# Performance work log

Measured on AMD Instinct MI355X. Metric: run time of the kernel, lower is better.

The kernel has to match this reference:

```python
import jax, jax.numpy as jnp
import numpy as np

BSZ, D = 64, 65536
N_NODES, N_FEATS, EMBED_DIM = 1024, 256, 256


def setup_inputs() -> dict:
    key = jax.random.key(0)
    k1, k2, k3, k4, k5, k6 = jax.random.split(key, 6)
    flat_inputs = jax.random.normal(k1, (BSZ, D), dtype=jnp.float32)
    node_ids = jax.random.randint(k2, (BSZ, D), 0, N_NODES, dtype=jnp.int64 if jax.config.jax_enable_x64 else jnp.int32)
    feat_ids = jax.random.randint(k3, (BSZ, D), 0, N_FEATS, dtype=jnp.int64 if jax.config.jax_enable_x64 else jnp.int32)
    # Linear(n_feats -> embed_dim): W is (embed_dim, n_feats) like torch, plus bias.
    lim = 1.0 / np.sqrt(N_FEATS)
    W = jax.random.uniform(k4, (EMBED_DIM, N_FEATS), minval=-lim, maxval=lim, dtype=jnp.float32)
    b = jax.random.uniform(k5, (EMBED_DIM,), minval=-lim, maxval=lim, dtype=jnp.float32)
    global_emb = jax.random.normal(k6, (N_NODES, EMBED_DIM), dtype=jnp.float32)
    return {"flat_inputs": flat_inputs, "node_ids": node_ids, "feat_ids": feat_ids,
            "W": W, "b": b, "global_emb": global_emb}


def _expand(vals, node_ids, feat_ids, n_nodes, n_feats):
    # scatter-fill a dense (bsz, n_nodes, n_feats) tensor (zeros elsewhere)
    bsz, d = vals.shape
    batch_ids = jnp.broadcast_to(jnp.arange(bsz)[:, None], (bsz, d))
    out = jnp.zeros((bsz, n_nodes, n_feats), dtype=vals.dtype)
    return out.at[batch_ids.ravel(), node_ids.ravel(), feat_ids.ravel()].set(vals.ravel())


def reference(flat_inputs, node_ids, feat_ids, W, b, global_emb):
    obs_mat = _expand(flat_inputs, node_ids, feat_ids, N_NODES, N_FEATS)
    mask_mat = _expand(jnp.ones_like(flat_inputs), node_ids, feat_ids, N_NODES, N_FEATS)
    obs_counts = mask_mat.sum(-1, keepdims=True)            # (bsz, n_nodes, 1)
    obs_masked = jnp.nan_to_num((obs_mat * mask_mat) / obs_counts)
    missing_node_mask = obs_counts == 0
    # nodewise Linear + global embedding broadcast over batch
    embedded = jnp.einsum('bnf,ef->bne', obs_masked, W) + b + global_emb[None, :, :]
    return embedded, missing_node_mask
```

## Files before the change

kernel.cpp:

```cpp
#include <hip/hip_runtime.h>
#include <hip/hip_bf16.h>

#define BSZ    64
#define DLEN   65536
#define NNODES 1024
#define NFEATS 256
#define EDIM   256
#define NROWS  (BSZ * NNODES)

#define NRANGE  32
#define NBUCKET (BSZ * NRANGE)
#define CHUNK   2048
#define LCAP    112
#define GCAP    2304
#define WPAD    268
#define HROWS   32

typedef __bf16 bf16x8 __attribute__((ext_vector_type(8)));
typedef float  f32x4  __attribute__((ext_vector_type(4)));

__device__ __forceinline__ unsigned short f2bf(float x) {
  union { float f; unsigned u; } c; c.f = x;
  unsigned r = c.u + 0x7FFFu + ((c.u >> 16) & 1u);
  return (unsigned short)(r >> 16);
}

__global__ __launch_bounds__(256) void wconv_kernel(
    const float* __restrict__ W, unsigned short* __restrict__ Wb,
    unsigned* __restrict__ gcnt) {
  int i = (blockIdx.x * 256 + threadIdx.x) * 4;
  float4 w = *(const float4*)(W + i);
  ushort4 o;
  o.x = f2bf(w.x); o.y = f2bf(w.y); o.z = f2bf(w.z); o.w = f2bf(w.w);
  *(ushort4*)(Wb + i) = o;
  if (blockIdx.x < 2)
    ((uint4*)gcnt)[blockIdx.x * 256 + threadIdx.x] = make_uint4(0u, 0u, 0u, 0u);
}

__global__ __launch_bounds__(512, 8) void bucket_kernel(
    const float* __restrict__ x, const int* __restrict__ nid,
    const int* __restrict__ fid, unsigned* __restrict__ gcnt,
    uint2* __restrict__ gbuf) {
  __shared__ uint2 lbuf[NRANGE][LCAP];
  __shared__ unsigned lcnt[NRANGE];
  __shared__ unsigned lbase[NRANGE];

  const int t = threadIdx.x;
  if (t < NRANGE) lcnt[t] = 0;
  __syncthreads();

  const int b = blockIdx.x >> 5;
  const int i = blockIdx.x * CHUNK + t * 4;

  float4 xv = *(const float4*)(x + i);
  int4   nv = *(const int4*)(nid + i);
  int4   fv = *(const int4*)(fid + i);
  int   nd[4] = {nv.x, nv.y, nv.z, nv.w};
  int   ft[4] = {fv.x, fv.y, fv.z, fv.w};
  float vl[4] = {xv.x, xv.y, xv.z, xv.w};
#pragma unroll
  for (int j = 0; j < 4; ++j) {
    int d = (i + j) & 0xFFFF;
    unsigned pack = (((unsigned)(d + 1)) << 15) | ((unsigned)f2bf(vl[j]) >> 1);
    int r = nd[j] >> 5;
    uint2 rec;
    rec.x = pack;
    rec.y = (unsigned)((nd[j] & 31) * WPAD + ft[j]);
    unsigned li = atomicAdd(&lcnt[r], 1u);
    if (li < LCAP) {
      lbuf[r][li] = rec;
    } else {
      unsigned gi = atomicAdd(&gcnt[b * NRANGE + r], 1u);
      if (gi < GCAP) gbuf[(size_t)(b * NRANGE + r) * GCAP + gi] = rec;
    }
  }
  __syncthreads();

  if (t < NRANGE) {
    unsigned n = lcnt[t]; if (n > LCAP) n = LCAP;
    lcnt[t] = n;
    lbase[t] = atomicAdd(&gcnt[b * NRANGE + t], n);
  }
  __syncthreads();

  const int wv = t >> 6, lane = t & 63;
#pragma unroll
  for (int rr = 0; rr < 4; ++rr) {
    int r = wv * 4 + rr;
    unsigned n  = lcnt[r];
    unsigned bs = lbase[r];
    uint2* dst = gbuf + (size_t)(b * NRANGE + r) * GCAP;
    for (unsigned j = lane; j < n; j += 64) {
      unsigned gi = bs + j;
      if (gi < GCAP) dst[gi] = lbuf[r][j];
    }
  }
}

__global__ __launch_bounds__(512, 8) void fused_kernel(
    const unsigned* __restrict__ gcnt, const uint2* __restrict__ gbuf,
    const unsigned short* __restrict__ Wb, const float* __restrict__ bias,
    const float* __restrict__ gemb,
    float* __restrict__ out_emb, float* __restrict__ out_mask) {
  __shared__ __align__(16) unsigned win[HROWS * WPAD];
  __shared__ float scl[HROWS];

  const int t = threadIdx.x;
  const int g = blockIdx.x;
  const int row0 = g * HROWS;
  const int nb = (g & 31) * HROWS;

  uint4* wz = (uint4*)win;
  for (int j = t; j < (HROWS * WPAD) / 4; j += 512) wz[j] = make_uint4(0u, 0u, 0u, 0u);
  __syncthreads();

  int cn = (int)gcnt[g]; if (cn > GCAP) cn = GCAP;
  const uint2* bk = gbuf + (size_t)g * GCAP;
  const uint4* bk4 = (const uint4*)bk;
  int np = cn >> 1;
  {
    uint4 r0, r1, r2;
    bool v0 = t < np, v1 = t + 512 < np, v2 = t + 1024 < np;
    if (v0) r0 = bk4[t];
    if (v1) r1 = bk4[t + 512];
    if (v2) r2 = bk4[t + 1024];
    if (v0) { atomicMax(&win[r0.y], r0.x); atomicMax(&win[r0.w], r0.z); }
    if (v1) { atomicMax(&win[r1.y], r1.x); atomicMax(&win[r1.w], r1.z); }
    if (v2) { atomicMax(&win[r2.y], r2.x); atomicMax(&win[r2.w], r2.z); }
    if ((cn & 1) && t == 0) {
      uint2 rec = bk[cn - 1];
      atomicMax(&win[rec.y], rec.x);
    }
  }
  __syncthreads();

  {
    const int lr  = t >> 4;
    const int seg = t & 15;
    const uint4* rowp = (const uint4*)&win[lr * WPAD];
    int c = 0;
#pragma unroll
    for (int j = 0; j < 4; ++j) {
      uint4 w = rowp[seg + 16 * j];
      c += (w.x != 0u) + (w.y != 0u) + (w.z != 0u) + (w.w != 0u);
    }
    c += __shfl_down(c, 8, 16);
    c += __shfl_down(c, 4, 16);
    c += __shfl_down(c, 2, 16);
    c += __shfl_down(c, 1, 16);
    if (seg == 0) {
      scl[lr] = c ? 1.0f / (float)c : 0.0f;
      out_mask[row0 + lr] = c ? 0.0f : 1.0f;
    }
  }

  const int wv   = t >> 6;
  const int lane = t & 63;
  const int cl   = lane & 15;
  const int q    = lane >> 4;
  const int col0 = wv * 32;

  f32x4 acc[2][2];
#pragma unroll
  for (int mt = 0; mt < 2; ++mt)
#pragma unroll
    for (int nt = 0; nt < 2; ++nt) acc[mt][nt] = (f32x4)(0.0f);

#pragma unroll
  for (int ks = 0; ks < 8; ++ks) {
    bf16x8 bfr[2];
#pragma unroll
    for (int nt = 0; nt < 2; ++nt) {
      const uint4* wp = (const uint4*)(Wb + (size_t)(col0 + nt * 16 + cl) * NFEATS + ks * 32 + q * 8);
      bfr[nt] = __builtin_bit_cast(bf16x8, *wp);
    }
#pragma unroll
    for (int mt = 0; mt < 2; ++mt) {
      const uint4* ap = (const uint4*)&win[(mt * 16 + cl) * WPAD + ks * 32 + q * 8];
      uint4 lo = ap[0], hi = ap[1];
      uint4 pk;
      pk.x = ((lo.x & 0x7FFFu) << 1) | ((lo.y & 0x7FFFu) << 17);
      pk.y = ((lo.z & 0x7FFFu) << 1) | ((lo.w & 0x7FFFu) << 17);
      pk.z = ((hi.x & 0x7FFFu) << 1) | ((hi.y & 0x7FFFu) << 17);
      pk.w = ((hi.z & 0x7FFFu) << 1) | ((hi.w & 0x7FFFu) << 17);
      bf16x8 afr = __builtin_bit_cast(bf16x8, pk);
#pragma unroll
      for (int nt = 0; nt < 2; ++nt)
        acc[mt][nt] = __builtin_amdgcn_mfma_f32_16x16x32_bf16(afr, bfr[nt], acc[mt][nt], 0, 0, 0);
    }
  }
  __syncthreads();

#pragma unroll
  for (int nt = 0; nt < 2; ++nt) {
    int col = col0 + nt * 16 + cl;
    float bv = bias[col];
#pragma unroll
    for (int mt = 0; mt < 2; ++mt) {
#pragma unroll
      for (int r2 = 0; r2 < 4; ++r2) {
        int row = mt * 16 + q * 4 + r2;
        float o = acc[mt][nt][r2] * scl[row] + bv + gemb[(size_t)(nb + row) * EDIM + col];
        out_emb[(size_t)(row0 + row) * EDIM + col] = o;
      }
    }
  }
}

extern "C" void kernel_launch(void* const* d_in, const int* in_sizes, int n_in,
                              void* d_out, int out_size, void* d_ws, size_t ws_size,
                              hipStream_t stream) {
  const float* x    = (const float*)d_in[0];
  const int*   nid  = (const int*)d_in[1];
  const int*   fid  = (const int*)d_in[2];
  const float* W    = (const float*)d_in[3];
  const float* bias = (const float*)d_in[4];
  const float* gemb = (const float*)d_in[5];

  float* out_emb  = (float*)d_out;
  float* out_mask = out_emb + (size_t)NROWS * EDIM;

  unsigned* gcnt = (unsigned*)d_ws;
  uint2* gbuf = (uint2*)((char*)d_ws + 8192);
  unsigned short* Wb = (unsigned short*)((char*)d_ws + 8192 + (size_t)NBUCKET * GCAP * sizeof(uint2));

  wconv_kernel<<<64, 256, 0, stream>>>(W, Wb, gcnt);
  bucket_kernel<<<(BSZ * DLEN) / CHUNK, 512, 0, stream>>>(x, nid, fid, gcnt, gbuf);
  fused_kernel<<<NBUCKET, 512, 0, stream>>>(gcnt, gbuf, Wb, bias, gemb, out_emb, out_mask);
}
```

Baseline: 159.9 us.

## Replace bucketing with direct global atomicMax into output buffer as scratch

The two-level bucket pipeline (shared-memory staging, then per-bucket global buffers, then shared-memory atomics) is replaced. The output embedding buffer is first zeroed and used as a dense (batch, node, feat) scratch grid. A scatter kernel then does one global atomicMax per input element into that grid, and the GEMM kernel loads its 32-row tile back into shared memory before overwriting the same rows with results. This removes the bucket counters, overflow handling and the intermediate record buffer. In exchange it adds a full-size zero pass and a full-size read-back of the output tensor, and it spreads 4M atomics across a grid far larger than L2.

```diff
diff --git a/kernel.cpp b/kernel.cpp
--- a/kernel.cpp
+++ b/kernel.cpp
@@ -8,13 +8,10 @@
 #define EDIM   256
 #define NROWS  (BSZ * NNODES)
 
-#define NRANGE  32
-#define NBUCKET (BSZ * NRANGE)
-#define CHUNK   2048
-#define LCAP    112
-#define GCAP    2304
-#define WPAD    268
-#define HROWS   32
+#define WPAD   268
+#define HROWS  32
+#define NBLK   (NROWS / HROWS)
+
 
 typedef __bf16 bf16x8 __attribute__((ext_vector_type(8)));
 typedef float  f32x4  __attribute__((ext_vector_type(4)));
@@ -25,80 +22,46 @@
   return (unsigned short)(r >> 16);
 }
 
-__global__ __launch_bounds__(256) void wconv_kernel(
+__global__ __launch_bounds__(256) void zero_wconv_kernel(
     const float* __restrict__ W, unsigned short* __restrict__ Wb,
-    unsigned* __restrict__ gcnt) {
-  int i = (blockIdx.x * 256 + threadIdx.x) * 4;
-  float4 w = *(const float4*)(W + i);
-  ushort4 o;
-  o.x = f2bf(w.x); o.y = f2bf(w.y); o.z = f2bf(w.z); o.w = f2bf(w.w);
-  *(ushort4*)(Wb + i) = o;
-  if (blockIdx.x < 2)
-    ((uint4*)gcnt)[blockIdx.x * 256 + threadIdx.x] = make_uint4(0u, 0u, 0u, 0u);
+    uint4* __restrict__ owin) {
+  const int t = threadIdx.x;
+  const int base = blockIdx.x * 1024 + t;
+#pragma unroll
+  for (int k = 0; k < 4; ++k)
+    owin[base + k * 256] = make_uint4(0u, 0u, 0u, 0u);
+  if (blockIdx.x < 64) {
+    int i = (blockIdx.x * 256 + t) * 4;
+    float4 w = *(const float4*)(W + i);
+    ushort4 o;
+    o.x = f2bf(w.x); o.y = f2bf(w.y); o.z = f2bf(w.z); o.w = f2bf(w.w);
+    *(ushort4*)(Wb + i) = o;
+  }
 }
 
-__global__ __launch_bounds__(512, 8) void bucket_kernel(
+__global__ __launch_bounds__(512, 8) void scatter_kernel(
     const float* __restrict__ x, const int* __restrict__ nid,
-    const int* __restrict__ fid, unsigned* __restrict__ gcnt,
-    uint2* __restrict__ gbuf) {
-  __shared__ uint2 lbuf[NRANGE][LCAP];
-  __shared__ unsigned lcnt[NRANGE];
-  __shared__ unsigned lbase[NRANGE];
-
+    const int* __restrict__ fid, unsigned* __restrict__ win) {
   const int t = threadIdx.x;
-  if (t < NRANGE) lcnt[t] = 0;
-  __syncthreads();
-
-  const int b = blockIdx.x >> 5;
-  const int i = blockIdx.x * CHUNK + t * 4;
+  const int i = (blockIdx.x * 512 + t) * 4;
 
   float4 xv = *(const float4*)(x + i);
   int4   nv = *(const int4*)(nid + i);
   int4   fv = *(const int4*)(fid + i);
+  const unsigned bb = (((unsigned)i >> 16) << 18);
   int   nd[4] = {nv.x, nv.y, nv.z, nv.w};
   int   ft[4] = {fv.x, fv.y, fv.z, fv.w};
   float vl[4] = {xv.x, xv.y, xv.z, xv.w};
 #pragma unroll
   for (int j = 0; j < 4; ++j) {
-    int d = (i + j) & 0xFFFF;
-    unsigned pack = (((unsigned)(d + 1)) << 15) | ((unsigned)f2bf(vl[j]) >> 1);
-    int r = nd[j] >> 5;
-    uint2 rec;
-    rec.x = pack;
-    rec.y = (unsigned)((nd[j] & 31) * WPAD + ft[j]);
-    unsigned li = atomicAdd(&lcnt[r], 1u);
-    if (li < LCAP) {
-      lbuf[r][li] = rec;
-    } else {
-      unsigned gi = atomicAdd(&gcnt[b * NRANGE + r], 1u);
-      if (gi < GCAP) gbuf[(size_t)(b * NRANGE + r) * GCAP + gi] = rec;
-    }
-  }
-  __syncthreads();
-
-  if (t < NRANGE) {
-    unsigned n = lcnt[t]; if (n > LCAP) n = LCAP;
-    lcnt[t] = n;
-    lbase[t] = atomicAdd(&gcnt[b * NRANGE + t], n);
-  }
-  __syncthreads();
-
-  const int wv = t >> 6, lane = t & 63;
-#pragma unroll
-  for (int rr = 0; rr < 4; ++rr) {
-    int r = wv * 4 + rr;
-    unsigned n  = lcnt[r];
-    unsigned bs = lbase[r];
-    uint2* dst = gbuf + (size_t)(b * NRANGE + r) * GCAP;
-    for (unsigned j = lane; j < n; j += 64) {
-      unsigned gi = bs + j;
-      if (gi < GCAP) dst[gi] = lbuf[r][j];
-    }
+    unsigned d = (unsigned)(i + j) & 0xFFFFu;
+    unsigned pack = ((d + 1u) << 15) | ((unsigned)f2bf(vl[j]) >> 1);
+    unsigned addr = bb | ((unsigned)nd[j] << 8) | (unsigned)ft[j];
+    atomicMax(win + addr, pack);
   }
 }
 
-__global__ __launch_bounds__(512, 8) void fused_kernel(
-    const unsigned* __restrict__ gcnt, const uint2* __restrict__ gbuf,
+__global__ __launch_bounds__(512, 8) void gemm_kernel(
     const unsigned short* __restrict__ Wb, const float* __restrict__ bias,
     const float* __restrict__ gemb,
     float* __restrict__ out_emb, float* __restrict__ out_mask) {
@@ -110,26 +73,15 @@
   const int row0 = g * HROWS;
   const int nb = (g & 31) * HROWS;
 
-  uint4* wz = (uint4*)win;
-  for (int j = t; j < (HROWS * WPAD) / 4; j += 512) wz[j] = make_uint4(0u, 0u, 0u, 0u);
-  __syncthreads();
-
-  int cn = (int)gcnt[g]; if (cn > GCAP) cn = GCAP;
-  const uint2* bk = gbuf + (size_t)g * GCAP;
-  const uint4* bk4 = (const uint4*)bk;
-  int np = cn >> 1;
   {
-    uint4 r0, r1, r2;
-    bool v0 = t < np, v1 = t + 512 < np, v2 = t + 1024 < np;
-    if (v0) r0 = bk4[t];
-    if (v1) r1 = bk4[t + 512];
-    if (v2) r2 = bk4[t + 1024];
-    if (v0) { atomicMax(&win[r0.y], r0.x); atomicMax(&win[r0.w], r0.z); }
-    if (v1) { atomicMax(&win[r1.y], r1.x); atomicMax(&win[r1.w], r1.z); }
-    if (v2) { atomicMax(&win[r2.y], r2.x); atomicMax(&win[r2.w], r2.z); }
-    if ((cn & 1) && t == 0) {
-      uint2 rec = bk[cn - 1];
-      atomicMax(&win[rec.y], rec.x);
+    const uint4* src = (const uint4*)out_emb + (size_t)row0 * 64;
+    uint4 v[4];
+#pragma unroll
+    for (int k = 0; k < 4; ++k) v[k] = src[t + k * 512];
+#pragma unroll
+    for (int k = 0; k < 4; ++k) {
+      int idx = t + k * 512;
+      *(uint4*)&win[(idx >> 6) * WPAD + (idx & 63) * 4] = v[k];
     }
   }
   __syncthreads();
@@ -220,11 +172,9 @@
   float* out_emb  = (float*)d_out;
   float* out_mask = out_emb + (size_t)NROWS * EDIM;
 
-  unsigned* gcnt = (unsigned*)d_ws;
-  uint2* gbuf = (uint2*)((char*)d_ws + 8192);
-  unsigned short* Wb = (unsigned short*)((char*)d_ws + 8192 + (size_t)NBUCKET * GCAP * sizeof(uint2));
+  unsigned short* Wb = (unsigned short*)d_ws;
 
-  wconv_kernel<<<64, 256, 0, stream>>>(W, Wb, gcnt);
-  bucket_kernel<<<(BSZ * DLEN) / CHUNK, 512, 0, stream>>>(x, nid, fid, gcnt, gbuf);
-  fused_kernel<<<NBUCKET, 512, 0, stream>>>(gcnt, gbuf, Wb, bias, gemb, out_emb, out_mask);
+  zero_wconv_kernel<<<4112, 256, 0, stream>>>(W, Wb, (uint4*)out_emb);
+  scatter_kernel<<<(BSZ * DLEN) / 2048, 512, 0, stream>>>(x, nid, fid, (unsigned*)out_emb);
+  gemm_kernel<<<NBLK, 512, 0, stream>>>(Wb, bias, gemb, out_emb, out_mask);
 }
```

Result: slower. 311.0 us (+94.5%).
